# Kernel tuning notes

Hardware: AMD Instinct MI355X
Metric: run time of the kernel (lower is better)

The kernel has to match this reference:

```python
import jax, jax.numpy as jnp
import numpy as np

N_NODES = 100000
N_EDGES = 1600000
D_IN = 128
D_OUT = 128

def setup_inputs() -> dict:
    key = jax.random.key(0)
    k1, k2, k3, k4, k5 = jax.random.split(key, 5)
    h = jax.random.normal(k1, (N_NODES, D_IN), dtype=jnp.float32)
    src = jax.random.randint(k2, (N_EDGES,), 0, N_NODES, dtype=jnp.int64)
    dst = jax.random.randint(k3, (N_EDGES,), 0, N_NODES, dtype=jnp.int64)
    # Xavier-ish init for the two linear maps (fc_self, fc_neigh), no bias
    scale = 1.0 / np.sqrt(D_IN)
    W_self = jax.random.normal(k4, (D_IN, D_OUT), dtype=jnp.float32) * scale
    W_neigh = jax.random.normal(k5, (D_IN, D_OUT), dtype=jnp.float32) * scale
    return {"h": h, "src": src, "dst": dst, "W_self": W_self, "W_neigh": W_neigh}

def reference(h, src, dst, W_self, W_neigh):
    # DGL SAGEConv mean aggregator, bias=False:
    #   h_neigh[v] = mean_{(u->v) in E} h[u]   (0 if v has no in-edges)
    #   out = h @ W_self + h_neigh @ W_neigh
    msg = h[src]  # [E, D_IN] neighbor gather
    neigh_sum = jax.ops.segment_sum(msg, dst, num_segments=N_NODES)  # [N, D_IN]
    deg = jax.ops.segment_sum(jnp.ones((src.shape[0],), dtype=h.dtype), dst,
                              num_segments=N_NODES)  # [N]
    h_neigh = neigh_sum / jnp.maximum(deg, 1.0)[:, None]
    return h @ W_self + h_neigh @ W_neigh
```

## Files before the change

kernel.cpp:

```cpp
#include <hip/hip_runtime.h>


constexpr int NN = 100000;
constexpr int NE = 1600000;
constexpr int D  = 128;
constexpr int BK = 64;
constexpr int NB = (NN + BK - 1) / BK;
constexpr int PB = 8192;
constexpr int CAPB = 2048;
constexpr int XST = 264;
constexpr int PADI = 32;
constexpr int PART_BLOCKS = (NE + PB - 1) / PB;
constexpr int WPK_BLOCKS  = 16;
constexpr int CVT_BLOCKS  = NN * D / 8 / 256;

typedef __attribute__((ext_vector_type(8))) short short8;
typedef __attribute__((ext_vector_type(4))) float floatx4;
typedef __attribute__((ext_vector_type(2))) float floatx2;

static __device__ __forceinline__ unsigned short f2bf(float f) {
    unsigned u = __float_as_uint(f);
    unsigned r = ((u >> 16) & 1u) + 0x7fffu;
    return (unsigned short)((u + r) >> 16);
}

__global__ __launch_bounds__(256) void k_prep(
    const float* __restrict__ h, const float* __restrict__ Wself,
    const float* __restrict__ Wneigh, const int* __restrict__ src,
    const int* __restrict__ dst, uint2* __restrict__ hf8,
    unsigned short* __restrict__ Wp, int* __restrict__ bcursor,
    unsigned* __restrict__ packed)
{
    const int t = threadIdx.x;
    if (blockIdx.x < PART_BLOCKS) {
        __shared__ int lh[NB];
        const int e0 = blockIdx.x * PB;
        for (int i = t; i < NB; i += 256) lh[i] = 0;
        __syncthreads();

        int myd[32], msrc[32];
#pragma unroll
        for (int j = 0; j < 32; ++j) {
            int e = e0 + j * 256 + t;
            myd[j] = (e < NE) ? dst[e] : -1;
        }
#pragma unroll
        for (int j = 0; j < 32; ++j) {
            int e = e0 + j * 256 + t;
            msrc[j] = (e < NE) ? src[e] : 0;
        }
#pragma unroll
        for (int j = 0; j < 32; ++j)
            if (myd[j] >= 0) atomicAdd(&lh[myd[j] >> 6], 1);
        __syncthreads();
        for (int i = t; i < NB; i += 256) {
            int c = lh[i];
            if (c) lh[i] = atomicAdd(&bcursor[(size_t)i * PADI], c);
        }
        __syncthreads();
#pragma unroll
        for (int j = 0; j < 32; ++j) {
            if (myd[j] >= 0) {
                int b = myd[j] >> 6;
                int pos = atomicAdd(&lh[b], 1);
                packed[(size_t)b * CAPB + pos] =
                    (unsigned)msrc[j] | ((unsigned)(myd[j] & 63) << 17);
            }
        }
    } else if (blockIdx.x < PART_BLOCKS + WPK_BLOCKS) {
        int kg  = (blockIdx.x - PART_BLOCKS) * 2 + (t >> 7);
        int col = t & 127;
        unsigned short v[8];
#pragma unroll
        for (int j = 0; j < 8; ++j) {
            int k = kg * 8 + j;
            const float* W = (k < 128) ? (Wself + (size_t)k * D)
                                       : (Wneigh + (size_t)(k - 128) * D);
            v[j] = f2bf(W[col]);
        }
        uint4 o;
        o.x = (unsigned)v[0] | ((unsigned)v[1] << 16);
        o.y = (unsigned)v[2] | ((unsigned)v[3] << 16);
        o.z = (unsigned)v[4] | ((unsigned)v[5] << 16);
        o.w = (unsigned)v[6] | ((unsigned)v[7] << 16);
        ((uint4*)Wp)[kg * 128 + col] = o;
    } else {
        int i = (blockIdx.x - PART_BLOCKS - WPK_BLOCKS) * 256 + t;
        const float4* h4 = (const float4*)h;
        float4 a = h4[(size_t)i * 2];
        float4 b = h4[(size_t)i * 2 + 1];
        unsigned q0 = __builtin_amdgcn_cvt_pk_fp8_f32(a.x, a.y, 0u, false);
        q0          = __builtin_amdgcn_cvt_pk_fp8_f32(a.z, a.w, q0, true);
        unsigned q1 = __builtin_amdgcn_cvt_pk_fp8_f32(b.x, b.y, 0u, false);
        q1          = __builtin_amdgcn_cvt_pk_fp8_f32(b.z, b.w, q1, true);
        hf8[i] = make_uint2(q0, q1);
    }
}

__global__ __launch_bounds__(512, 6) void k_agg_gemm(
    const float* __restrict__ h, const uint2* __restrict__ hf8,
    const int* __restrict__ bcursor, const unsigned* __restrict__ packed,
    const unsigned short* __restrict__ Wp, float* __restrict__ out)
{
    __shared__ unsigned short Xs[BK][XST];
    __shared__ unsigned sorted[CAPB];
    __shared__ int cnt[BK], offs[BK], cur[BK];

    const int t      = threadIdx.x;
    const int bucket = blockIdx.x;
    const size_t ebeg = (size_t)bucket * CAPB;
    const int ecnt   = min(bcursor[(size_t)bucket * PADI], CAPB);

    if (t < BK) cnt[t] = 0;

    {
        int row = t >> 3, seg = t & 7;
        int grow = min(bucket * BK + row, NN - 1);
        const float4* hp = (const float4*)(h + (size_t)grow * D + seg * 16);
        float4 f0 = hp[0], f1 = hp[1], f2 = hp[2], f3 = hp[3];
        uint4 q0, q1;
        q0.x = (unsigned)f2bf(f0.x) | ((unsigned)f2bf(f0.y) << 16);
        q0.y = (unsigned)f2bf(f0.z) | ((unsigned)f2bf(f0.w) << 16);
        q0.z = (unsigned)f2bf(f1.x) | ((unsigned)f2bf(f1.y) << 16);
        q0.w = (unsigned)f2bf(f1.z) | ((unsigned)f2bf(f1.w) << 16);
        q1.x = (unsigned)f2bf(f2.x) | ((unsigned)f2bf(f2.y) << 16);
        q1.y = (unsigned)f2bf(f2.z) | ((unsigned)f2bf(f2.w) << 16);
        q1.z = (unsigned)f2bf(f3.x) | ((unsigned)f2bf(f3.y) << 16);
        q1.w = (unsigned)f2bf(f3.z) | ((unsigned)f2bf(f3.w) << 16);
        *(uint4*)&Xs[row][seg * 16]     = q0;
        *(uint4*)&Xs[row][seg * 16 + 8] = q1;
    }
    __syncthreads();

    unsigned pk[4];
#pragma unroll
    for (int i = 0; i < 4; ++i) {
        int idx = t + i * 512;
        pk[i] = (idx < ecnt) ? packed[ebeg + idx] : 0u;
    }
#pragma unroll
    for (int i = 0; i < 4; ++i) {
        int idx = t + i * 512;
        if (idx < ecnt) atomicAdd(&cnt[(pk[i] >> 17) & 63u], 1);
    }
    __syncthreads();
    if (t < BK) {
        int v = cnt[t];
        int sum = v;
#pragma unroll
        for (int off = 1; off < 64; off <<= 1) {
            int u = __shfl_up(sum, off, 64);
            if (t >= off) sum += u;
        }
        offs[t] = sum - v;
        cur[t]  = sum - v;
    }
    __syncthreads();
#pragma unroll
    for (int i = 0; i < 4; ++i) {
        int idx = t + i * 512;
        if (idx < ecnt) {
            int pos = atomicAdd(&cur[(pk[i] >> 17) & 63u], 1);
            sorted[pos] = pk[i] & 0x1FFFFu;
        }
    }
    __syncthreads();

    const int slot = t >> 4;
    const int l16  = t & 15;
#pragma unroll
    for (int ni = 0; ni < 2; ++ni) {
        int node = slot + ni * 32;
        const int beg = offs[node];
        const int n   = cnt[node];
        float a0[8] = {0,0,0,0,0,0,0,0};
        float a1[8] = {0,0,0,0,0,0,0,0};
        int e = 0;
        for (; e + 3 < n; e += 4) {
            uint2 x0 = hf8[(size_t)sorted[beg + e]     * 16 + l16];
            uint2 x1 = hf8[(size_t)sorted[beg + e + 1] * 16 + l16];
            uint2 x2 = hf8[(size_t)sorted[beg + e + 2] * 16 + l16];
            uint2 x3 = hf8[(size_t)sorted[beg + e + 3] * 16 + l16];
#pragma unroll
            for (int half = 0; half < 2; ++half) {
                unsigned w0 = half ? x0.y : x0.x, w1 = half ? x1.y : x1.x;
                unsigned w2 = half ? x2.y : x2.x, w3 = half ? x3.y : x3.x;
                floatx2 p;
                p = __builtin_amdgcn_cvt_pk_f32_fp8(w0, false); a0[half*4+0]+=p.x; a0[half*4+1]+=p.y;
                p = __builtin_amdgcn_cvt_pk_f32_fp8(w0, true);  a0[half*4+2]+=p.x; a0[half*4+3]+=p.y;
                p = __builtin_amdgcn_cvt_pk_f32_fp8(w1, false); a1[half*4+0]+=p.x; a1[half*4+1]+=p.y;
                p = __builtin_amdgcn_cvt_pk_f32_fp8(w1, true);  a1[half*4+2]+=p.x; a1[half*4+3]+=p.y;
                p = __builtin_amdgcn_cvt_pk_f32_fp8(w2, false); a0[half*4+0]+=p.x; a0[half*4+1]+=p.y;
                p = __builtin_amdgcn_cvt_pk_f32_fp8(w2, true);  a0[half*4+2]+=p.x; a0[half*4+3]+=p.y;
                p = __builtin_amdgcn_cvt_pk_f32_fp8(w3, false); a1[half*4+0]+=p.x; a1[half*4+1]+=p.y;
                p = __builtin_amdgcn_cvt_pk_f32_fp8(w3, true);  a1[half*4+2]+=p.x; a1[half*4+3]+=p.y;
            }
        }
        for (; e < n; ++e) {
            uint2 x = hf8[(size_t)sorted[beg + e] * 16 + l16];
#pragma unroll
            for (int half = 0; half < 2; ++half) {
                unsigned w = half ? x.y : x.x;
                floatx2 p;
                p = __builtin_amdgcn_cvt_pk_f32_fp8(w, false); a0[half*4+0]+=p.x; a0[half*4+1]+=p.y;
                p = __builtin_amdgcn_cvt_pk_f32_fp8(w, true);  a0[half*4+2]+=p.x; a0[half*4+3]+=p.y;
            }
        }
        float inv = (n > 0) ? 1.0f / (float)n : 0.0f;
        unsigned short m[8];
#pragma unroll
        for (int j = 0; j < 8; ++j)
            m[j] = f2bf((a0[j] + a1[j]) * inv);
        uint4 o;
        o.x = (unsigned)m[0] | ((unsigned)m[1] << 16);
        o.y = (unsigned)m[2] | ((unsigned)m[3] << 16);
        o.z = (unsigned)m[4] | ((unsigned)m[5] << 16);
        o.w = (unsigned)m[6] | ((unsigned)m[7] << 16);
        *(uint4*)&Xs[node][128 + l16 * 8] = o;
    }
    __syncthreads();

    const int wave  = t >> 6;
    const int lane  = t & 63;
    const int wl16  = lane & 15;
    const int kg4   = lane >> 4;
    const int wrow  = wave & 3;
    const int chalf = wave >> 2;
    floatx4 acc[4];
#pragma unroll
    for (int c = 0; c < 4; ++c) acc[c] = (floatx4){0.f, 0.f, 0.f, 0.f};

    const int arow = wrow * 16 + wl16;
#pragma unroll
    for (int ks = 0; ks < 8; ++ks) {
        const short8 a = *(const short8*)&Xs[arow][ks * 32 + kg4 * 8];
#pragma unroll
        for (int c = 0; c < 4; ++c) {
            const int ct = chalf * 4 + c;
            const short8 b = *(const short8*)(Wp + (((ks * 4 + kg4) * 128) + ct * 16 + wl16) * 8);
            acc[c] = __builtin_amdgcn_mfma_f32_16x16x32_bf16(a, b, acc[c], 0, 0, 0);
        }
    }

    const int rbase = bucket * BK + wrow * 16 + kg4 * 4;
#pragma unroll
    for (int r = 0; r < 4; ++r) {
        int row = rbase + r;
        if (row < NN) {
            float* o = out + (size_t)row * D + chalf * 64 + wl16;
#pragma unroll
            for (int c = 0; c < 4; ++c)
                o[c * 16] = acc[c][r];
        }
    }
}

extern "C" void kernel_launch(void* const* d_in, const int* in_sizes, int n_in,
                              void* d_out, int out_size, void* d_ws, size_t ws_size,
                              hipStream_t stream) {
    const float* h      = (const float*)d_in[0];
    const int*   src    = (const int*)d_in[1];
    const int*   dst    = (const int*)d_in[2];
    const float* Wself  = (const float*)d_in[3];
    const float* Wneigh = (const float*)d_in[4];
    float*       out    = (float*)d_out;

    uint2* hf8         = (uint2*)d_ws;
    unsigned short* Wp = (unsigned short*)(hf8 + (size_t)NN * D / 8);
    unsigned* packed   = (unsigned*)(Wp + 256 * D);
    uintptr_t bc_a     = ((uintptr_t)(packed + (size_t)NB * CAPB) + 255) & ~(uintptr_t)255;
    int* bcursor       = (int*)bc_a;

    hipMemsetAsync(bcursor, 0, (size_t)NB * PADI * sizeof(int), stream);

    k_prep     <<<dim3(PART_BLOCKS + WPK_BLOCKS + CVT_BLOCKS), 256, 0, stream>>>(
                   h, Wself, Wneigh, src, dst, hf8, Wp, bcursor, packed);
    k_agg_gemm <<<dim3(NB), 512, 0, stream>>>(h, hf8, bcursor, packed, Wp, out);
}
```

Baseline: 183.4 us.

## Widen neighbor gather to 16-byte loads with 8 lanes per node

```diff
diff --git a/kernel.cpp b/kernel.cpp
--- a/kernel.cpp
+++ b/kernel.cpp
@@ -7,8 +7,8 @@
 constexpr int BK = 64;
 constexpr int NB = (NN + BK - 1) / BK;
 constexpr int PB = 8192;
-constexpr int CAPB = 2048;
-constexpr int XST = 264;
+constexpr int CAPB = 1536;
+constexpr int XST = 258;
 constexpr int PADI = 32;
 constexpr int PART_BLOCKS = (NE + PB - 1) / PB;
 constexpr int WPK_BLOCKS  = 16;
@@ -63,8 +63,9 @@
             if (myd[j] >= 0) {
                 int b = myd[j] >> 6;
                 int pos = atomicAdd(&lh[b], 1);
-                packed[(size_t)b * CAPB + pos] =
-                    (unsigned)msrc[j] | ((unsigned)(myd[j] & 63) << 17);
+                if (pos < CAPB)
+                    packed[(size_t)b * CAPB + pos] =
+                        (unsigned)msrc[j] | ((unsigned)(myd[j] & 63) << 17);
             }
         }
     } else if (blockIdx.x < PART_BLOCKS + WPK_BLOCKS) {
@@ -132,14 +133,14 @@
     }
     __syncthreads();
 
-    unsigned pk[4];
-#pragma unroll
-    for (int i = 0; i < 4; ++i) {
+    unsigned pk[3];
+#pragma unroll
+    for (int i = 0; i < 3; ++i) {
         int idx = t + i * 512;
         pk[i] = (idx < ecnt) ? packed[ebeg + idx] : 0u;
     }
 #pragma unroll
-    for (int i = 0; i < 4; ++i) {
+    for (int i = 0; i < 3; ++i) {
         int idx = t + i * 512;
         if (idx < ecnt) atomicAdd(&cnt[(pk[i] >> 17) & 63u], 1);
     }
@@ -157,7 +158,7 @@
     }
     __syncthreads();
 #pragma unroll
-    for (int i = 0; i < 4; ++i) {
+    for (int i = 0; i < 3; ++i) {
         int idx = t + i * 512;
         if (idx < ecnt) {
             int pos = atomicAdd(&cur[(pk[i] >> 17) & 63u], 1);
@@ -166,57 +167,71 @@
     }
     __syncthreads();
 
-    const int slot = t >> 4;
-    const int l16  = t & 15;
-#pragma unroll
-    for (int ni = 0; ni < 2; ++ni) {
-        int node = slot + ni * 32;
-        const int beg = offs[node];
-        const int n   = cnt[node];
-        float a0[8] = {0,0,0,0,0,0,0,0};
-        float a1[8] = {0,0,0,0,0,0,0,0};
+    {
+        const int g  = t >> 3;
+        const int l8 = t & 7;
+        const int beg = offs[g];
+        const int n   = cnt[g];
+        const uint4* __restrict__ hr = (const uint4*)hf8;
+
+        floatx2 ac[8];
+#pragma unroll
+        for (int j = 0; j < 8; ++j) ac[j] = (floatx2){0.f, 0.f};
+
+#define ACC16(X) do {                                                         \
+            unsigned ww0 = (X).x, ww1 = (X).y, ww2 = (X).z, ww3 = (X).w;      \
+            ac[0] += __builtin_amdgcn_cvt_pk_f32_fp8(ww0, false);             \
+            ac[1] += __builtin_amdgcn_cvt_pk_f32_fp8(ww0, true);              \
+            ac[2] += __builtin_amdgcn_cvt_pk_f32_fp8(ww1, false);             \
+            ac[3] += __builtin_amdgcn_cvt_pk_f32_fp8(ww1, true);              \
+            ac[4] += __builtin_amdgcn_cvt_pk_f32_fp8(ww2, false);             \
+            ac[5] += __builtin_amdgcn_cvt_pk_f32_fp8(ww2, true);              \
+            ac[6] += __builtin_amdgcn_cvt_pk_f32_fp8(ww3, false);             \
+            ac[7] += __builtin_amdgcn_cvt_pk_f32_fp8(ww3, true);              \
+        } while (0)
+
         int e = 0;
-        for (; e + 3 < n; e += 4) {
-            uint2 x0 = hf8[(size_t)sorted[beg + e]     * 16 + l16];
-            uint2 x1 = hf8[(size_t)sorted[beg + e + 1] * 16 + l16];
-            uint2 x2 = hf8[(size_t)sorted[beg + e + 2] * 16 + l16];
-            uint2 x3 = hf8[(size_t)sorted[beg + e + 3] * 16 + l16];
-#pragma unroll
-            for (int half = 0; half < 2; ++half) {
-                unsigned w0 = half ? x0.y : x0.x, w1 = half ? x1.y : x1.x;
-                unsigned w2 = half ? x2.y : x2.x, w3 = half ? x3.y : x3.x;
-                floatx2 p;
-                p = __builtin_amdgcn_cvt_pk_f32_fp8(w0, false); a0[half*4+0]+=p.x; a0[half*4+1]+=p.y;
-                p = __builtin_amdgcn_cvt_pk_f32_fp8(w0, true);  a0[half*4+2]+=p.x; a0[half*4+3]+=p.y;
-                p = __builtin_amdgcn_cvt_pk_f32_fp8(w1, false); a1[half*4+0]+=p.x; a1[half*4+1]+=p.y;
-                p = __builtin_amdgcn_cvt_pk_f32_fp8(w1, true);  a1[half*4+2]+=p.x; a1[half*4+3]+=p.y;
-                p = __builtin_amdgcn_cvt_pk_f32_fp8(w2, false); a0[half*4+0]+=p.x; a0[half*4+1]+=p.y;
-                p = __builtin_amdgcn_cvt_pk_f32_fp8(w2, true);  a0[half*4+2]+=p.x; a0[half*4+3]+=p.y;
-                p = __builtin_amdgcn_cvt_pk_f32_fp8(w3, false); a1[half*4+0]+=p.x; a1[half*4+1]+=p.y;
-                p = __builtin_amdgcn_cvt_pk_f32_fp8(w3, true);  a1[half*4+2]+=p.x; a1[half*4+3]+=p.y;
-            }
-        }
-        for (; e < n; ++e) {
-            uint2 x = hf8[(size_t)sorted[beg + e] * 16 + l16];
-#pragma unroll
-            for (int half = 0; half < 2; ++half) {
-                unsigned w = half ? x.y : x.x;
-                floatx2 p;
-                p = __builtin_amdgcn_cvt_pk_f32_fp8(w, false); a0[half*4+0]+=p.x; a0[half*4+1]+=p.y;
-                p = __builtin_amdgcn_cvt_pk_f32_fp8(w, true);  a0[half*4+2]+=p.x; a0[half*4+3]+=p.y;
-            }
-        }
+        for (; e + 7 < n; e += 8) {
+            uint4 x0 = hr[(size_t)sorted[beg + e]     * 8 + l8];
+            uint4 x1 = hr[(size_t)sorted[beg + e + 1] * 8 + l8];
+            uint4 x2 = hr[(size_t)sorted[beg + e + 2] * 8 + l8];
+            uint4 x3 = hr[(size_t)sorted[beg + e + 3] * 8 + l8];
+            uint4 x4 = hr[(size_t)sorted[beg + e + 4] * 8 + l8];
+            uint4 x5 = hr[(size_t)sorted[beg + e + 5] * 8 + l8];
+            uint4 x6 = hr[(size_t)sorted[beg + e + 6] * 8 + l8];
+            uint4 x7 = hr[(size_t)sorted[beg + e + 7] * 8 + l8];
+            ACC16(x0); ACC16(x1); ACC16(x2); ACC16(x3);
+            ACC16(x4); ACC16(x5); ACC16(x6); ACC16(x7);
+        }
+        for (; e + 1 < n; e += 2) {
+            uint4 x0 = hr[(size_t)sorted[beg + e]     * 8 + l8];
+            uint4 x1 = hr[(size_t)sorted[beg + e + 1] * 8 + l8];
+            ACC16(x0); ACC16(x1);
+        }
+        if (e < n) {
+            uint4 x0 = hr[(size_t)sorted[beg + e] * 8 + l8];
+            ACC16(x0);
+        }
+#undef ACC16
+
         float inv = (n > 0) ? 1.0f / (float)n : 0.0f;
-        unsigned short m[8];
-#pragma unroll
-        for (int j = 0; j < 8; ++j)
-            m[j] = f2bf((a0[j] + a1[j]) * inv);
-        uint4 o;
-        o.x = (unsigned)m[0] | ((unsigned)m[1] << 16);
-        o.y = (unsigned)m[2] | ((unsigned)m[3] << 16);
-        o.z = (unsigned)m[4] | ((unsigned)m[5] << 16);
-        o.w = (unsigned)m[6] | ((unsigned)m[7] << 16);
-        *(uint4*)&Xs[node][128 + l16 * 8] = o;
+        unsigned short m[16];
+#pragma unroll
+        for (int j = 0; j < 8; ++j) {
+            m[j * 2]     = f2bf(ac[j].x * inv);
+            m[j * 2 + 1] = f2bf(ac[j].y * inv);
+        }
+        uint4 o0, o1;
+        o0.x = (unsigned)m[0]  | ((unsigned)m[1]  << 16);
+        o0.y = (unsigned)m[2]  | ((unsigned)m[3]  << 16);
+        o0.z = (unsigned)m[4]  | ((unsigned)m[5]  << 16);
+        o0.w = (unsigned)m[6]  | ((unsigned)m[7]  << 16);
+        o1.x = (unsigned)m[8]  | ((unsigned)m[9]  << 16);
+        o1.y = (unsigned)m[10] | ((unsigned)m[11] << 16);
+        o1.z = (unsigned)m[12] | ((unsigned)m[13] << 16);
+        o1.w = (unsigned)m[14] | ((unsigned)m[15] << 16);
+        *(uint4*)&Xs[g][128 + l8 * 16]     = o0;
+        *(uint4*)&Xs[g][128 + l8 * 16 + 8] = o1;
     }
     __syncthreads();
 
```

Result: slower. 314.7 us (+71.6%).
